# Kernel optimization log

Measured on AMD Instinct MI355X. Metric: run time of the kernel, lower is better.

Reference implementation:

```python
import jax, jax.numpy as jnp
import numpy as np

IN_F, OUT_F, TOKENS = 4096, 11008, 4096


def setup_inputs() -> dict:
    key = jax.random.key(0)
    k1, k2, k3, k4, k5 = jax.random.split(key, 5)
    x = jax.random.normal(k1, (TOKENS, IN_F), dtype=jnp.float32)
    # uint8-range quantized weights stored as int32 (harness dtype constraint)
    weight_quant = jax.random.randint(k2, (OUT_F, IN_F), 0, 255, dtype=jnp.int32)
    # per-output-channel scale (small positive) and zero-point near mid-range
    scale = jax.random.uniform(k3, (OUT_F,), dtype=jnp.float32) * 0.02 + 0.001
    zero = jax.random.uniform(k4, (OUT_F,), dtype=jnp.float32) * 255.0
    bias = jax.random.normal(k5, (OUT_F,), dtype=jnp.float32)
    return {"x": x, "weight_quant": weight_quant, "scale": scale, "zero": zero, "bias": bias}


def reference(x, weight_quant, scale, zero, bias):
    # dequantize per output channel: W = (W_q - zero) * scale, shape [out, in]
    W = (weight_quant.astype(jnp.float32) - zero[:, None]) * scale[:, None]
    # y = x @ W^T + bias -> [tokens, out]
    return jnp.einsum('ti,oi->to', x, W) + bias
```

## Files before the change

kernel.cpp:

```cpp
#include <hip/hip_runtime.h>

typedef unsigned short u16;
typedef unsigned int   u32;
typedef unsigned long long u64;
typedef signed char    i8;

typedef int   i32x4 __attribute__((ext_vector_type(4)));

#define IN_F   4096
#define OUT_F  11008
#define TOKENS 4096

#define BM 256
#define BN 256
#define BKQ 128
#define MT (TOKENS / BM)
#define NT (OUT_F / BN)
#define KTILES (IN_F / BKQ)

#define GLOAD_LDS16(g, l)                                                        \
    __builtin_amdgcn_global_load_lds(                                            \
        (const __attribute__((address_space(1))) u32*)(u64)(g),                  \
        (__attribute__((address_space(3))) u32*)(u64)(l), 16, 0, 0)

#define BAR() __builtin_amdgcn_s_barrier()
#define VM(N) asm volatile("s_waitcnt vmcnt(" #N ")" ::: "memory")

__device__ __forceinline__ int pack4(int a, int b, int c, int d) {
    return (a & 255) | ((b & 255) << 8) | ((c & 255) << 16) | (d << 24);
}

__global__ __launch_bounds__(256) void prep_x_kernel(
    const float* __restrict__ x, i8* __restrict__ xq,
    float* __restrict__ rowsum, float* __restrict__ rowscale) {
    const int row = blockIdx.x;
    const int tid = threadIdx.x;
    const float4* xr = reinterpret_cast<const float4*>(x + (size_t)row * IN_F);
    float4 v[4];
    float s = 0.f, mx = 0.f;
#pragma unroll
    for (int i = 0; i < 4; ++i) {
        v[i] = xr[tid * 4 + i];
        s += v[i].x + v[i].y + v[i].z + v[i].w;
        mx = fmaxf(mx, fmaxf(fmaxf(fabsf(v[i].x), fabsf(v[i].y)),
                             fmaxf(fabsf(v[i].z), fabsf(v[i].w))));
    }
#pragma unroll
    for (int off = 32; off > 0; off >>= 1) {
        s += __shfl_down(s, off, 64);
        mx = fmaxf(mx, __shfl_down(mx, off, 64));
    }
    __shared__ float ss[4], sm[4];
    if ((tid & 63) == 0) { ss[tid >> 6] = s; sm[tid >> 6] = mx; }
    __syncthreads();
    const float tot = ss[0] + ss[1] + ss[2] + ss[3];
    const float m4  = fmaxf(fmaxf(sm[0], sm[1]), fmaxf(sm[2], sm[3]));
    const float mg  = fmaxf(m4, 1e-20f);
    const float inv = 127.0f / mg;
    if (tid == 0) { rowsum[row] = tot; rowscale[row] = mg * (1.0f / 127.0f); }
    int4 o;
    int q[16];
#pragma unroll
    for (int i = 0; i < 4; ++i) {
        q[4 * i + 0] = (int)rintf(v[i].x * inv);
        q[4 * i + 1] = (int)rintf(v[i].y * inv);
        q[4 * i + 2] = (int)rintf(v[i].z * inv);
        q[4 * i + 3] = (int)rintf(v[i].w * inv);
    }
    o.x = pack4(q[0], q[1], q[2], q[3]);
    o.y = pack4(q[4], q[5], q[6], q[7]);
    o.z = pack4(q[8], q[9], q[10], q[11]);
    o.w = pack4(q[12], q[13], q[14], q[15]);
    reinterpret_cast<int4*>(xq + (size_t)row * IN_F)[tid] = o;
}

__global__ __launch_bounds__(256) void prep_w_kernel(
    const int* __restrict__ wq, i8* __restrict__ wb) {
    const size_t total16 = (size_t)OUT_F * IN_F / 16;
    size_t i = (size_t)blockIdx.x * blockDim.x + threadIdx.x;
    const size_t stride = (size_t)gridDim.x * blockDim.x;
    const int4* p = reinterpret_cast<const int4*>(wq);
    int4* o = reinterpret_cast<int4*>(wb);
    for (; i < total16; i += stride) {
        int4 a = p[i * 4], b = p[i * 4 + 1], c = p[i * 4 + 2], d = p[i * 4 + 3];
        int4 v;
        v.x = pack4(a.x - 128, a.y - 128, a.z - 128, a.w - 128);
        v.y = pack4(b.x - 128, b.y - 128, b.z - 128, b.w - 128);
        v.z = pack4(c.x - 128, c.y - 128, c.z - 128, c.w - 128);
        v.w = pack4(d.x - 128, d.y - 128, d.z - 128, d.w - 128);
        o[i] = v;
    }
}


#define LDA_HALF(P, MH)                                                           \
    _Pragma("unroll") for (int m = 0; m < 4; ++m)                                 \
    _Pragma("unroll") for (int s = 0; s < 2; ++s)                                 \
        af[m][s] = *(const i32x4*)((const char*)&AS[P][0] +                       \
            ((wr * 128 + (MH) * 64 + m * 16 + l15) * 128 +                        \
             (((s * 4 + kq) ^ (l15 & 7)) << 4)));

#define LDB_HALF(P, NH)                                                           \
    _Pragma("unroll") for (int n = 0; n < 2; ++n)                                 \
    _Pragma("unroll") for (int s = 0; s < 2; ++s)                                 \
        bfr[(NH) * 2 + n][s] = *(const i32x4*)((const char*)&BS[P][0] +           \
            ((wc * 64 + (NH) * 32 + n * 16 + l15) * 128 +                         \
             (((s * 4 + kq) ^ (l15 & 7)) << 4)));

#define MFMA_Q(MH, NH)                                                            \
    __builtin_amdgcn_s_setprio(1);                                                \
    _Pragma("unroll") for (int m = 0; m < 4; ++m)                                 \
    _Pragma("unroll") for (int n = 0; n < 2; ++n)                                 \
    _Pragma("unroll") for (int s = 0; s < 2; ++s)                                 \
        acc[(MH) * 4 + m][(NH) * 2 + n] = __builtin_amdgcn_mfma_i32_16x16x64_i8(  \
            af[m][s], bfr[(NH) * 2 + n][s], acc[(MH) * 4 + m][(NH) * 2 + n],      \
            0, 0, 0);                                                             \
    __builtin_amdgcn_s_setprio(0);

#define STAGE_A(P, H, KT) {                                                       \
    _Pragma("unroll") for (int j = 0; j < 2; ++j) {                               \
        const int i_ = 2 * w + j;                                                 \
        const int chunk = (((H) * 8 + (i_ & 7) + ((i_ >> 3) << 4)) << 10);        \
        const int row_ = (chunk + lane * 16) >> 7;                                \
        const int cb_ = (((lane & 7) ^ (row_ & 7)) << 4);                         \
        const i8* g_ = Abase + (size_t)row_ * IN_F + (KT) * BKQ + cb_;            \
        GLOAD_LDS16(g_, (char*)&AS[P][0] + chunk);                                \
    } }

#define STAGE_B(P, H, KT) {                                                       \
    _Pragma("unroll") for (int j = 0; j < 2; ++j) {                               \
        const int i_ = 2 * w + j;                                                 \
        const int chunk = (((H) * 4 + (i_ & 3) + ((i_ >> 2) << 3)) << 10);        \
        const int row_ = (chunk + lane * 16) >> 7;                                \
        const int cb_ = (((lane & 7) ^ (row_ & 7)) << 4);                         \
        const i8* g_ = Bbase + (size_t)row_ * IN_F + (KT) * BKQ + cb_;            \
        GLOAD_LDS16(g_, (char*)&BS[P][0] + chunk);                                \
    } }

__global__ __launch_bounds__(512, 1) void qgemm_kernel(
    const i8* __restrict__ Xq, const i8* __restrict__ Wqb,
    const float* __restrict__ rowsum, const float* __restrict__ rowscale,
    const float* __restrict__ scale, const float* __restrict__ zero,
    const float* __restrict__ bias, float* __restrict__ out) {
    __shared__ i8 AS[2][BM * BKQ];
    __shared__ i8 BS[2][BN * BKQ];

    const int bid = blockIdx.x;
    const int xcd = bid & 7;
    const int g   = bid >> 3;
    const int mt  = xcd * 2 + (g & 1);
    const int nt  = g >> 1;

    const int tid  = threadIdx.x;
    const int w    = tid >> 6;
    const int lane = tid & 63;
    const int wr   = w >> 2;
    const int wc   = w & 3;
    const int l15  = lane & 15;
    const int kq   = lane >> 4;

    const i8* Abase = Xq  + (size_t)mt * BM * IN_F;
    const i8* Bbase = Wqb + (size_t)nt * BN * IN_F;

    i32x4 af[4][2];
    i32x4 bfr[4][2];
    i32x4 acc[8][4];
    const i32x4 zi = {0, 0, 0, 0};
#pragma unroll
    for (int m = 0; m < 8; ++m)
#pragma unroll
        for (int n = 0; n < 4; ++n) acc[m][n] = zi;

    STAGE_A(0, 0, 0);
    STAGE_B(0, 0, 0);
    STAGE_B(0, 1, 0);
    STAGE_A(0, 1, 0);
    STAGE_A(1, 0, 1);
    STAGE_B(1, 0, 1);
    STAGE_B(1, 1, 1);
    VM(10);
    BAR();

    for (int i = 0; i < 15; ++i) {
        const int t = 2 * i;
        LDA_HALF(0, 0); LDB_HALF(0, 0);
        STAGE_A(1, 1, t + 1);
        BAR();
        MFMA_Q(0, 0);
        VM(10); BAR();
        LDB_HALF(0, 1);
        STAGE_A(0, 0, t + 2);
        BAR();
        MFMA_Q(0, 1);
        VM(10); BAR();
        LDA_HALF(0, 1);
        STAGE_B(0, 0, t + 2);
        BAR();
        MFMA_Q(1, 0);
        BAR();
        STAGE_B(0, 1, t + 2);
        BAR();
        MFMA_Q(1, 1);
        VM(10); BAR();
        LDA_HALF(1, 0); LDB_HALF(1, 0);
        STAGE_A(0, 1, t + 2);
        BAR();
        MFMA_Q(0, 0);
        VM(10); BAR();
        LDB_HALF(1, 1);
        STAGE_A(1, 0, t + 3);
        BAR();
        MFMA_Q(0, 1);
        VM(10); BAR();
        LDA_HALF(1, 1);
        STAGE_B(1, 0, t + 3);
        BAR();
        MFMA_Q(1, 0);
        BAR();
        STAGE_B(1, 1, t + 3);
        BAR();
        MFMA_Q(1, 1);
        VM(10); BAR();
    }

    LDA_HALF(0, 0); LDB_HALF(0, 0);
    STAGE_A(1, 1, 31);
    BAR();
    MFMA_Q(0, 0);
    VM(10); BAR();
    LDB_HALF(0, 1);
    BAR();
    MFMA_Q(0, 1);
    VM(8); BAR();
    LDA_HALF(0, 1);
    BAR();
    MFMA_Q(1, 0);
    BAR();
    BAR();
    MFMA_Q(1, 1);
    VM(4); BAR();
    LDA_HALF(1, 0); LDB_HALF(1, 0);
    BAR();
    MFMA_Q(0, 0);
    VM(2); BAR();
    LDB_HALF(1, 1);
    BAR();
    MFMA_Q(0, 1);
    VM(0); BAR();
    LDA_HALF(1, 1);
    BAR();
    MFMA_Q(1, 0);
    BAR();
    BAR();
    MFMA_Q(1, 1);

    const int rowt = mt * BM + wr * 128;
    const int colt = nt * BN + wc * 64;

    float scn[4], bcn[4], ccn[4];
#pragma unroll
    for (int n = 0; n < 4; ++n) {
        const int col = colt + n * 16 + l15;
        scn[n] = scale[col];
        bcn[n] = scn[n] * (128.0f - zero[col]);
        ccn[n] = bias[col];
    }
#pragma unroll
    for (int m = 0; m < 8; ++m) {
#pragma unroll
        for (int j = 0; j < 4; ++j) {
            const int r = rowt + m * 16 + kq * 4 + j;
            const float rsv = rowsum[r];
            const float sxv = rowscale[r];
#pragma unroll
            for (int n = 0; n < 4; ++n) {
                out[(size_t)r * OUT_F + colt + n * 16 + l15] =
                    scn[n] * (sxv * (float)acc[m][n][j]) + bcn[n] * rsv + ccn[n];
            }
        }
    }
}

extern "C" void kernel_launch(void* const* d_in, const int* in_sizes, int n_in,
                              void* d_out, int out_size, void* d_ws, size_t ws_size,
                              hipStream_t stream) {
    const float* x     = (const float*)d_in[0];
    const int*   wq    = (const int*)d_in[1];
    const float* scale = (const float*)d_in[2];
    const float* zero  = (const float*)d_in[3];
    const float* bias  = (const float*)d_in[4];
    float* out = (float*)d_out;

    char* ws = (char*)d_ws;
    i8* Wqb = (i8*)ws;
    i8* Xq  = (i8*)(ws + (size_t)OUT_F * IN_F);
    float* rowsum   = (float*)(ws + (size_t)OUT_F * IN_F + (size_t)TOKENS * IN_F);
    float* rowscale = rowsum + TOKENS;

    prep_w_kernel<<<2048, 256, 0, stream>>>(wq, Wqb);
    prep_x_kernel<<<TOKENS, 256, 0, stream>>>(x, Xq, rowsum, rowscale);
    qgemm_kernel<<<MT * NT, 512, 0, stream>>>(Xq, Wqb, rowsum, rowscale,
                                              scale, zero, bias, out);
}
```

Baseline: 239.9 us.

## Shrink GEMM tile to 256x128 with K=64 and run two 256-thread blocks per CU

```diff
diff --git a/kernel.cpp b/kernel.cpp
--- a/kernel.cpp
+++ b/kernel.cpp
@@ -12,8 +12,8 @@
 #define TOKENS 4096
 
 #define BM 256
-#define BN 256
-#define BKQ 128
+#define BN 128
+#define BKQ 64
 #define MT (TOKENS / BM)
 #define NT (OUT_F / BN)
 #define KTILES (IN_F / BKQ)
@@ -95,49 +95,41 @@
 
 #define LDA_HALF(P, MH)                                                           \
     _Pragma("unroll") for (int m = 0; m < 4; ++m)                                 \
-    _Pragma("unroll") for (int s = 0; s < 2; ++s)                                 \
-        af[m][s] = *(const i32x4*)((const char*)&AS[P][0] +                       \
-            ((wr * 128 + (MH) * 64 + m * 16 + l15) * 128 +                        \
-             (((s * 4 + kq) ^ (l15 & 7)) << 4)));
+        af[m] = *(const i32x4*)((const char*)&AS[P][0] +                          \
+            ((wr * 128 + (MH) * 64 + m * 16 + l15) * 64 +                         \
+             ((kq ^ ((l15 >> 1) & 3)) << 4)));
 
 #define LDB_HALF(P, NH)                                                           \
     _Pragma("unroll") for (int n = 0; n < 2; ++n)                                 \
-    _Pragma("unroll") for (int s = 0; s < 2; ++s)                                 \
-        bfr[(NH) * 2 + n][s] = *(const i32x4*)((const char*)&BS[P][0] +           \
-            ((wc * 64 + (NH) * 32 + n * 16 + l15) * 128 +                         \
-             (((s * 4 + kq) ^ (l15 & 7)) << 4)));
+        bfr[(NH) * 2 + n] = *(const i32x4*)((const char*)&BS[P][0] +              \
+            ((wc * 64 + (NH) * 32 + n * 16 + l15) * 64 +                          \
+             ((kq ^ ((l15 >> 1) & 3)) << 4)));
 
 #define MFMA_Q(MH, NH)                                                            \
     __builtin_amdgcn_s_setprio(1);                                                \
     _Pragma("unroll") for (int m = 0; m < 4; ++m)                                 \
     _Pragma("unroll") for (int n = 0; n < 2; ++n)                                 \
-    _Pragma("unroll") for (int s = 0; s < 2; ++s)                                 \
         acc[(MH) * 4 + m][(NH) * 2 + n] = __builtin_amdgcn_mfma_i32_16x16x64_i8(  \
-            af[m][s], bfr[(NH) * 2 + n][s], acc[(MH) * 4 + m][(NH) * 2 + n],      \
-            0, 0, 0);                                                             \
+            af[m], bfr[(NH) * 2 + n], acc[(MH) * 4 + m][(NH) * 2 + n], 0, 0, 0);  \
     __builtin_amdgcn_s_setprio(0);
 
 #define STAGE_A(P, H, KT) {                                                       \
     _Pragma("unroll") for (int j = 0; j < 2; ++j) {                               \
         const int i_ = 2 * w + j;                                                 \
-        const int chunk = (((H) * 8 + (i_ & 7) + ((i_ >> 3) << 4)) << 10);        \
-        const int row_ = (chunk + lane * 16) >> 7;                                \
-        const int cb_ = (((lane & 7) ^ (row_ & 7)) << 4);                         \
-        const i8* g_ = Abase + (size_t)row_ * IN_F + (KT) * BKQ + cb_;            \
+        const int chunk = (((H) * 4 + (i_ & 3) + ((i_ >> 2) << 3)) << 10);        \
+        const int row_ = (chunk + lane * 16) >> 6;                                \
+        const i8* g_ = Abase + (size_t)row_ * IN_F + (KT) * BKQ + sa;             \
         GLOAD_LDS16(g_, (char*)&AS[P][0] + chunk);                                \
     } }
 
 #define STAGE_B(P, H, KT) {                                                       \
-    _Pragma("unroll") for (int j = 0; j < 2; ++j) {                               \
-        const int i_ = 2 * w + j;                                                 \
-        const int chunk = (((H) * 4 + (i_ & 3) + ((i_ >> 2) << 3)) << 10);        \
-        const int row_ = (chunk + lane * 16) >> 7;                                \
-        const int cb_ = (((lane & 7) ^ (row_ & 7)) << 4);                         \
-        const i8* g_ = Bbase + (size_t)row_ * IN_F + (KT) * BKQ + cb_;            \
+        const int chunk = (((H) * 2 + (w & 1) + ((w >> 1) << 2)) << 10);          \
+        const int row_ = (chunk + lane * 16) >> 6;                                \
+        const i8* g_ = Bbase + (size_t)row_ * IN_F + (KT) * BKQ + sa;             \
         GLOAD_LDS16(g_, (char*)&BS[P][0] + chunk);                                \
-    } }
-
-__global__ __launch_bounds__(512, 1) void qgemm_kernel(
+    }
+
+__global__ __launch_bounds__(256, 2) void qgemm_kernel(
     const i8* __restrict__ Xq, const i8* __restrict__ Wqb,
     const float* __restrict__ rowsum, const float* __restrict__ rowscale,
     const float* __restrict__ scale, const float* __restrict__ zero,
@@ -154,16 +146,17 @@
     const int tid  = threadIdx.x;
     const int w    = tid >> 6;
     const int lane = tid & 63;
-    const int wr   = w >> 2;
-    const int wc   = w & 3;
+    const int wr   = w >> 1;
+    const int wc   = w & 1;
     const int l15  = lane & 15;
     const int kq   = lane >> 4;
+    const int sa = (((lane & 3) ^ ((lane >> 3) & 3)) << 4);
 
     const i8* Abase = Xq  + (size_t)mt * BM * IN_F;
     const i8* Bbase = Wqb + (size_t)nt * BN * IN_F;
 
-    i32x4 af[4][2];
-    i32x4 bfr[4][2];
+    i32x4 af[4];
+    i32x4 bfr[4];
     i32x4 acc[8][4];
     const i32x4 zi = {0, 0, 0, 0};
 #pragma unroll
@@ -178,21 +171,21 @@
     STAGE_A(1, 0, 1);
     STAGE_B(1, 0, 1);
     STAGE_B(1, 1, 1);
-    VM(10);
-    BAR();
-
-    for (int i = 0; i < 15; ++i) {
+    VM(4);
+    BAR();
+
+    for (int i = 0; i < 31; ++i) {
         const int t = 2 * i;
         LDA_HALF(0, 0); LDB_HALF(0, 0);
         STAGE_A(1, 1, t + 1);
         BAR();
         MFMA_Q(0, 0);
-        VM(10); BAR();
+        BAR();
         LDB_HALF(0, 1);
         STAGE_A(0, 0, t + 2);
         BAR();
         MFMA_Q(0, 1);
-        VM(10); BAR();
+        BAR();
         LDA_HALF(0, 1);
         STAGE_B(0, 0, t + 2);
         BAR();
@@ -201,17 +194,17 @@
         STAGE_B(0, 1, t + 2);
         BAR();
         MFMA_Q(1, 1);
-        VM(10); BAR();
+        VM(4); BAR();
         LDA_HALF(1, 0); LDB_HALF(1, 0);
         STAGE_A(0, 1, t + 2);
         BAR();
         MFMA_Q(0, 0);
-        VM(10); BAR();
+        BAR();
         LDB_HALF(1, 1);
         STAGE_A(1, 0, t + 3);
         BAR();
         MFMA_Q(0, 1);
-        VM(10); BAR();
+        BAR();
         LDA_HALF(1, 1);
         STAGE_B(1, 0, t + 3);
         BAR();
@@ -220,33 +213,33 @@
         STAGE_B(1, 1, t + 3);
         BAR();
         MFMA_Q(1, 1);
-        VM(10); BAR();
+        VM(4); BAR();
     }
 
     LDA_HALF(0, 0); LDB_HALF(0, 0);
-    STAGE_A(1, 1, 31);
+    STAGE_A(1, 1, 63);
     BAR();
     MFMA_Q(0, 0);
-    VM(10); BAR();
+    BAR();
     LDB_HALF(0, 1);
     BAR();
     MFMA_Q(0, 1);
-    VM(8); BAR();
+    BAR();
     LDA_HALF(0, 1);
     BAR();
     MFMA_Q(1, 0);
     BAR();
     BAR();
     MFMA_Q(1, 1);
-    VM(4); BAR();
+    VM(0); BAR();
     LDA_HALF(1, 0); LDB_HALF(1, 0);
     BAR();
     MFMA_Q(0, 0);
-    VM(2); BAR();
+    BAR();
     LDB_HALF(1, 1);
     BAR();
     MFMA_Q(0, 1);
-    VM(0); BAR();
+    BAR();
     LDA_HALF(1, 1);
     BAR();
     MFMA_Q(1, 0);
@@ -299,6 +292,6 @@
 
     prep_w_kernel<<<2048, 256, 0, stream>>>(wq, Wqb);
     prep_x_kernel<<<TOKENS, 256, 0, stream>>>(x, Xq, rowsum, rowscale);
-    qgemm_kernel<<<MT * NT, 512, 0, stream>>>(Xq, Wqb, rowsum, rowscale,
+    qgemm_kernel<<<MT * NT, 256, 0, stream>>>(Xq, Wqb, rowsum, rowscale,
                                               scale, zero, bias, out);
 }
```

After: 264.0 us. +10.0%, slower.
